# Kernel tuning notes

Measured on AMD Instinct MI355X. Metric: run time of the kernel, lower is better.

The kernel has to match this reference:

```python
import jax, jax.numpy as jnp
from jax import lax
import numpy as np

WINDOW_SIZES = (5, 9, 15)
BASE_LOWER, BASE_UPPER = 0.05, 0.2

def _conv3x3(x, w, b):
    # NCHW / OIHW, stride 1, SAME zero padding (torch Conv2d padding=1)
    y = lax.conv_general_dilated(x, w, (1, 1), 'SAME',
                                 dimension_numbers=('NCHW', 'OIHW', 'NCHW'))
    return y + b.reshape(1, -1, 1, 1)

def _leaky(x):
    return jnp.where(x >= 0, x, 0.2 * x)

def _box_mean(f, win):
    # Depthwise uniform box filter with reflect padding == mean over unfold patches.
    B, C, H, W = f.shape
    pad = win // 2
    fp = jnp.pad(f, ((0, 0), (0, 0), (pad, pad), (pad, pad)), mode='reflect')
    k = jnp.full((C, 1, win, win), 1.0 / (win * win), f.dtype)
    return lax.conv_general_dilated(fp, k, (1, 1), 'VALID',
                                    dimension_numbers=('NCHW', 'OIHW', 'NCHW'),
                                    feature_group_count=C)

def _std_map(features, win):
    m = _box_mean(features, win)                      # E[x]
    m2 = _box_mean(features * features, win)          # E[x^2]
    var = jnp.maximum(m2 - m * m, 0.0)                # == mean((x - mean)^2)
    std = jnp.sqrt(var + 1e-8)                        # [B, C, H, W]
    return jnp.mean(std, axis=1, keepdims=True)       # [B, 1, H, W]

def _forward(x, conv1_w, conv1_b, conv2_w, conv2_b, conv3_w, conv3_b,
             channel_weights, fusion_w, fusion_b):
    # feature extractor: 4 -> 32 -> 16 -> 8
    f = _leaky(_conv3x3(x, conv1_w, conv1_b))
    f = _leaky(_conv3x3(f, conv2_w, conv2_b))
    f = _conv3x3(f, conv3_w, conv3_b)                 # [B, 8, H, W]

    maps = [_std_map(f, w) for w in WINDOW_SIZES]
    multi = jnp.concatenate(maps, axis=1)             # [B, 3, H, W]
    # 1x1 conv fusion (3 -> 1)
    fused = jnp.einsum('bshw,os->bohw', multi, fusion_w[:, :, 0, 0]) \
            + fusion_b.reshape(1, -1, 1, 1)           # [B, 1, H, W]

    # adaptive thresholds (torch.std is unbiased -> ddof=1)
    global_std = jnp.std(x, axis=(2, 3), keepdims=True, ddof=1)   # [B, 4, 1, 1]
    global_factor = jnp.clip(global_std * 5.0, 0.5, 2.0)
    lower = BASE_LOWER * global_factor
    upper = BASE_UPPER * global_factor
    cw = jax.nn.softmax(channel_weights).reshape(1, -1, 1, 1)
    channel_std = jnp.std(x * cw, axis=(2, 3), keepdims=True, ddof=1)
    channel_factor = jnp.clip(channel_std * 2.0, 0.8, 1.2)
    lower = lower * channel_factor                    # [B, 4, 1, 1]
    upper = upper * channel_factor

    ns = jnp.clip((fused - lower) / (upper - lower), 0.0, 1.0)  # broadcasts to [B,4,H,W]
    return jax.nn.sigmoid(6.0 * ns - 3.0)

def setup_inputs() -> dict:
    key = jax.random.key(0)
    ks = jax.random.split(key, 10)
    B, C, H, W = 4, 4, 1024, 1024
    def w_init(k, shape):
        fan_in = shape[1] * shape[2] * shape[3]
        return jax.random.normal(k, shape, jnp.float32) / np.float32(np.sqrt(fan_in))
    return {
        'x': jax.random.uniform(ks[0], (B, C, H, W), jnp.float32),
        'conv1_w': w_init(ks[1], (32, 4, 3, 3)),
        'conv1_b': jax.random.normal(ks[2], (32,), jnp.float32) * 0.01,
        'conv2_w': w_init(ks[3], (16, 32, 3, 3)),
        'conv2_b': jax.random.normal(ks[4], (16,), jnp.float32) * 0.01,
        'conv3_w': w_init(ks[5], (8, 16, 3, 3)),
        'conv3_b': jax.random.normal(ks[6], (8,), jnp.float32) * 0.01,
        'channel_weights': jnp.ones((4,), jnp.float32) / 4.0,
        'fusion_w': w_init(ks[7], (1, 3, 1, 1)),
        'fusion_b': jax.random.normal(ks[8], (1,), jnp.float32) * 0.01,
    }

def reference(x, conv1_w, conv1_b, conv2_w, conv2_b, conv3_w, conv3_b,
              channel_weights, fusion_w, fusion_b):
    return _forward(x, conv1_w, conv1_b, conv2_w, conv2_b, conv3_w, conv3_b,
                    channel_weights, fusion_w, fusion_b)
```

## Files before the change

### kernel.cpp

```cpp
#include <hip/hip_runtime.h>
#include <math.h>

#define H 1024
#define W 1024
#define HW (H * W)

typedef _Float16 half8 __attribute__((ext_vector_type(8)));
typedef _Float16 half4 __attribute__((ext_vector_type(4)));
typedef _Float16 h2 __attribute__((ext_vector_type(2)));
typedef float f32x4 __attribute__((ext_vector_type(4)));
typedef unsigned uint4v __attribute__((ext_vector_type(4)));

__device__ __forceinline__ float fast_sqrtf(float x) { return __builtin_amdgcn_sqrtf(x); }
__device__ __forceinline__ float fast_expf(float x) { return __builtin_amdgcn_exp2f(x * 1.44269504088896340736f); }

__device__ __forceinline__ h2 pkrtz(float a, float b) {
    return __builtin_bit_cast(h2, __builtin_amdgcn_cvt_pkrtz(a, b));
}

__global__ __launch_bounds__(256) void stats_partial(const float* __restrict__ x,
                                                     double* __restrict__ part) {
    int blk = blockIdx.x;
    int bc = blk >> 5;
    int j = blk & 31;
    const float* p = x + (size_t)bc * HW + (size_t)j * (HW / 32);
    int tid = threadIdx.x;
    double s = 0.0, q = 0.0;
    const float4* p4 = (const float4*)p;
    for (int i = tid; i < (HW / 32) / 4; i += 256) {
        float4 v = p4[i];
        s += (double)v.x + (double)v.y + (double)v.z + (double)v.w;
        q += (double)v.x * v.x + (double)v.y * v.y + (double)v.z * v.z + (double)v.w * v.w;
    }
    __shared__ double ls[256], lq[256];
    ls[tid] = s;
    lq[tid] = q;
    __syncthreads();
    for (int ofs = 128; ofs > 0; ofs >>= 1) {
        if (tid < ofs) { ls[tid] += ls[tid + ofs]; lq[tid] += lq[tid + ofs]; }
        __syncthreads();
    }
    if (tid == 0) {
        part[blk * 2] = ls[0];
        part[blk * 2 + 1] = lq[0];
    }
}

__global__ __launch_bounds__(256) void stats_final_prep(const double* __restrict__ part,
                                                        const float* __restrict__ chw,
                                                        const float* __restrict__ w1,
                                                        const float* __restrict__ w2,
                                                        const float* __restrict__ w3,
                                                        float* __restrict__ stats,
                                                        _Float16* __restrict__ w1a,
                                                        _Float16* __restrict__ w3f,
                                                        _Float16* __restrict__ w2bh) {
    int tid = threadIdx.x;
    __shared__ float cw[4];
    if (tid == 0) {
        float m = fmaxf(fmaxf(chw[0], chw[1]), fmaxf(chw[2], chw[3]));
        float e0 = expf(chw[0] - m), e1 = expf(chw[1] - m);
        float e2 = expf(chw[2] - m), e3 = expf(chw[3] - m);
        float s = e0 + e1 + e2 + e3;
        cw[0] = e0 / s; cw[1] = e1 / s; cw[2] = e2 / s; cw[3] = e3 / s;
    }
    __syncthreads();
    if (tid < 16) {
        double s = 0.0, q = 0.0;
        for (int j = 0; j < 32; j++) {
            s += part[(tid * 32 + j) * 2];
            q += part[(tid * 32 + j) * 2 + 1];
        }
        double n = (double)HW;
        double var = (q - s * s / n) / (n - 1.0);
        if (var < 0) var = 0;
        float gs = (float)sqrt(var);
        int c = tid & 3;
        float gf = fminf(fmaxf(gs * 5.0f, 0.5f), 2.0f);
        float cf = fminf(fmaxf(gs * cw[c] * 2.0f, 0.8f), 1.2f);
        stats[tid * 2] = 0.05f * gf * cf;
        stats[tid * 2 + 1] = 0.20f * gf * cf;
    }
    for (int i = tid; i < 256; i += 256) {
        int s = i >> 6, l = i & 63;
        int c = s >> 1, h = s & 1;
        int m = l & 15, cg = l >> 4;
        int co = h * 16 + m;
#pragma unroll
        for (int j = 0; j < 8; j++) {
            int k = c * 32 + cg * 8 + j;
            float v = 0.f;
            if (k < 36) {
                int t = k >> 2, ci = k & 3;
                v = w1[(co * 4 + ci) * 9 + t];
            }
            w1a[i * 8 + j] = (_Float16)v;
        }
    }
    for (int idx = tid; idx < 576; idx += 256) {
        int t = idx >> 6, l = idx & 63;
        int co = l & 15, cg = l >> 4;
#pragma unroll
        for (int j = 0; j < 8; j++) {
            int ci = cg * 8 + j;
            w2bh[idx * 8 + j] = (_Float16)w2[(co * 32 + ci) * 9 + t];
        }
    }
    for (int idx = tid; idx < 384; idx += 256) {
        int t = idx >> 6, l = idx & 63;
        int ky = t / 2, grp = t & 1;
        int co = l & 15, bq = l >> 4;
#pragma unroll
        for (int j = 0; j < 8; j++) {
            int k = bq * 8 + j;
            float v = 0.f;
            if (co < 8) {
                if (grp == 0) {
                    int kxp = k >> 4, ci = k & 15;
                    v = w3[((co * 16 + ci) * 3 + ky) * 3 + kxp];
                } else if (k < 16) {
                    v = w3[((co * 16 + k) * 3 + ky) * 3 + 2];
                }
            }
            w3f[idx * 8 + j] = (_Float16)v;
        }
    }
}

__global__ __launch_bounds__(256, 5) void conv12_mfma(const float* __restrict__ x,
                                                      const _Float16* __restrict__ w1a,
                                                      const float* __restrict__ b1,
                                                      const _Float16* __restrict__ wbh,
                                                      const float* __restrict__ b2,
                                                      _Float16* __restrict__ f2n,
                                                      size_t f2n_bstride, int batch0) {
    __shared__ __align__(16) char smem[30656];
    char* f1t = smem;
    unsigned* xp = (unsigned*)(smem + 27200);
    int tid = threadIdx.x;
    int lane = tid & 63;
    int wid = tid >> 6;
    int bx = blockIdx.x * 32, by = blockIdx.y * 8;
    int n = lane & 15, cg = lane >> 4;
    int m = lane & 15, b = lane >> 4;
    const float* xb = x + (size_t)(batch0 + blockIdx.z) * 4 * HW;
    _Float16* f2nb = f2n + (size_t)blockIdx.z * f2n_bstride;

    {
        int idx = tid;
        int r = tid / 36, c = tid - r * 36, plane = 0;
#pragma unroll
        for (int it = 0; it < 4; ++it) {
            if (idx < 864) {
                int gy = by + r - 2, gx = bx + c - 2;
                float v0 = 0.f, v1 = 0.f;
                if ((unsigned)gy < H && (unsigned)gx < W) {
                    const float* pp = xb + (size_t)(2 * plane) * HW + gy * W + gx;
                    v0 = pp[0];
                    v1 = pp[HW];
                }
                xp[idx] = __builtin_bit_cast(unsigned, pkrtz(v0, v1));
            }
            idx += 256;
            c += 4; if (c >= 36) { c -= 36; r += 1; }
            r += 7; if (r >= 12) { r -= 12; plane += 1; }
        }
    }

    half8 Wf00 = *(const half8*)(w1a + (0 * 64 + lane) * 8);
    half8 Wf01 = *(const half8*)(w1a + (1 * 64 + lane) * 8);
    half8 Wf10 = *(const half8*)(w1a + (2 * 64 + lane) * 8);
    half8 Wf11 = *(const half8*)(w1a + (3 * 64 + lane) * 8);
    float bias1[8];
#pragma unroll
    for (int h = 0; h < 2; h++)
#pragma unroll
        for (int j = 0; j < 4; j++)
            bias1[h * 4 + j] = b1[h * 16 + cg * 4 + j];
    half8 Bh[9];
#pragma unroll
    for (int t = 0; t < 9; t++)
        Bh[t] = *(const half8*)(wbh + (t * 64 + lane) * 8);
    f32x4 binit;
#pragma unroll
    for (int j = 0; j < 4; j++) binit[j] = b2[b * 4 + j];

    int t0 = 2 * cg, t1 = 2 * cg + 1;
    int dy0 = (t0 * 11) >> 5, dx0 = t0 - 3 * dy0;
    int dy1 = (t1 * 11) >> 5, dx1 = t1 - 3 * dy1;
    int off0 = dy0 * 36 + dx0, off1 = dy1 * 36 + dx1;
    __syncthreads();

#pragma unroll 1
    for (int tt = wid; tt < 22; tt += 4) {
        int p = tt * 16 + n;
        bool valid = p < 340;
        int pc = valid ? p : 339;
        int ry = pc / 34, cx = pc - ry * 34;
        int gy = by + ry - 1, gx = bx + cx - 1;
        bool ok = ((unsigned)gy < H) && ((unsigned)gx < W);
        int base = ry * 36 + cx;
        uint4v uv;
        uv.x = xp[base + off0];
        uv.y = xp[432 + base + off0];
        uv.z = xp[base + off1];
        uv.w = xp[432 + base + off1];
        half8 Xh0 = __builtin_bit_cast(half8, uv);
        half8 Xh1 = {0, 0, 0, 0, 0, 0, 0, 0};
        if (cg == 0) {
            uint4v uw = {0, 0, 0, 0};
            uw.x = xp[base + 74];
            uw.y = xp[432 + base + 74];
            Xh1 = __builtin_bit_cast(half8, uw);
        }
        f32x4 d0, d1;
#pragma unroll
        for (int j = 0; j < 4; j++) { d0[j] = bias1[j]; d1[j] = bias1[4 + j]; }
        d0 = __builtin_amdgcn_mfma_f32_16x16x32_f16(Wf00, Xh0, d0, 0, 0, 0);
        d0 = __builtin_amdgcn_mfma_f32_16x16x32_f16(Wf10, Xh1, d0, 0, 0, 0);
        d1 = __builtin_amdgcn_mfma_f32_16x16x32_f16(Wf01, Xh0, d1, 0, 0, 0);
        d1 = __builtin_amdgcn_mfma_f32_16x16x32_f16(Wf11, Xh1, d1, 0, 0, 0);
        if (valid) {
            char* pxb = f1t + ry * 2720 + cx * 80;
#pragma unroll
            for (int h = 0; h < 2; h++) {
                f32x4 d = h ? d1 : d0;
                half4 hq;
#pragma unroll
                for (int j = 0; j < 4; j++) {
                    float v = d[j];
                    v = fmaxf(v, 0.2f * v);
                    v = ok ? v : 0.f;
                    hq[j] = (_Float16)v;
                }
                *(half4*)(pxb + (h * 4 + cg) * 8) = hq;
            }
        }
    }
    __syncthreads();

    int wx = wid & 1, wy = wid >> 1;
    f32x4 acc2[4];
#pragma unroll
    for (int r = 0; r < 4; r++) acc2[r] = binit;
#pragma unroll
    for (int iy = 0; iy < 6; iy++) {
        int f1row = wy * 4 + iy;
        half8 ah[3];
#pragma unroll
        for (int kx = 0; kx < 3; kx++) {
            int pxi = wx * 16 + m + kx;
            ah[kx] = *(const half8*)(f1t + f1row * 2720 + pxi * 80 + b * 16);
        }
#pragma unroll
        for (int kx = 0; kx < 3; kx++) {
#pragma unroll
            for (int ry = 0; ry < 4; ry++) {
                if (ry >= iy - 2 && ry <= iy) {
                    const int t = (iy - ry) * 3 + kx;
                    acc2[ry] = __builtin_amdgcn_mfma_f32_16x16x32_f16(Bh[t], ah[kx], acc2[ry], 0, 0, 0);
                }
            }
        }
    }

    int x0 = bx + wx * 16 + m;
    int y0 = by + wy * 4;
    int co_off = b * 4;
#pragma unroll
    for (int ry = 0; ry < 4; ry++) {
        half4 hq;
#pragma unroll
        for (int j = 0; j < 4; j++) {
            float v = acc2[ry][j];
            v = fmaxf(v, 0.2f * v);
            hq[j] = (_Float16)v;
        }
        *(half4*)(f2nb + ((size_t)(y0 + ry) * W + x0) * 16 + co_off) = hq;
    }
}

__global__ __launch_bounds__(256) void conv3_mfma(const _Float16* __restrict__ f2n,
                                                  size_t f2n_bstride, int batch0,
                                                  const _Float16* __restrict__ w3f,
                                                  const float* __restrict__ bias,
                                                  _Float16* __restrict__ f3all) {
    __shared__ __align__(16) char st[10 * 34 * 40];
    int tid = threadIdx.x;
    int lane = tid & 63;
    int wid = tid >> 6;
    int bx = blockIdx.x * 32, by = blockIdx.y * 8;
    const _Float16* f2nb = f2n + (size_t)blockIdx.z * f2n_bstride;
    _Float16* f3 = f3all + (size_t)(batch0 + blockIdx.z) * 8 * HW;

    for (int idx = tid; idx < 680; idx += 256) {
        int c0 = idx & 1;
        int rp = idx >> 1;
        int r = rp / 34, p = rp - r * 34;
        int gy = by + r - 1, gx = bx + p - 1;
        half8 v = {0, 0, 0, 0, 0, 0, 0, 0};
        if ((unsigned)gy < H && (unsigned)gx < W)
            v = *(const half8*)(f2nb + ((size_t)gy * W + gx) * 16 + c0 * 8);
        *(half8*)(st + r * 1360 + p * 40 + c0 * 16) = v;
    }

    half8 F0[3], F1[3];
#pragma unroll
    for (int ky = 0; ky < 3; ky++) {
        F0[ky] = *(const half8*)(w3f + ((ky * 2 + 0) * 64 + lane) * 8);
        F1[ky] = *(const half8*)(w3f + ((ky * 2 + 1) * 64 + lane) * 8);
    }
    int m = lane & 15, b = lane >> 4;
    int halfco = b & 1, kxp = b >> 1;
    int wx = wid & 1, wy = wid >> 1;
    float bc = (m < 8) ? bias[m] : 0.f;
    f32x4 acc[4];
#pragma unroll
    for (int r = 0; r < 4; r++) acc[r] = (f32x4){bc, bc, bc, bc};
    int pA = wx * 16 + m + kxp;
    int pB = wx * 16 + m + 2;
    __syncthreads();

#pragma unroll
    for (int iy = 0; iy < 6; iy++) {
        const char* rp = st + (wy * 4 + iy) * 1360;
        half8 ka_h = *(const half8*)(rp + pA * 40 + halfco * 16);
        half8 kb_h = *(const half8*)(rp + pB * 40 + halfco * 16);
#pragma unroll
        for (int ry = 0; ry < 4; ry++) {
            if (ry >= iy - 2 && ry <= iy) {
                const int ky = iy - ry;
                acc[ry] = __builtin_amdgcn_mfma_f32_16x16x32_f16(ka_h, F0[ky], acc[ry], 0, 0, 0);
                acc[ry] = __builtin_amdgcn_mfma_f32_16x16x32_f16(kb_h, F1[ky], acc[ry], 0, 0, 0);
            }
        }
    }

    if (m < 8) {
#pragma unroll
        for (int ry = 0; ry < 4; ry++) {
            int y = by + wy * 4 + ry;
            half4 hv = {(_Float16)acc[ry][0], (_Float16)acc[ry][1],
                        (_Float16)acc[ry][2], (_Float16)acc[ry][3]};
            *(half4*)(f3 + (size_t)m * HW + (size_t)y * W + bx + wx * 16 + b * 4) = hv;
        }
    }
}

__global__ __launch_bounds__(256) void stdfuse_fused(const _Float16* __restrict__ f3all,
                                                     const float* __restrict__ fw,
                                                     const float* __restrict__ fb,
                                                     const float* __restrict__ stats,
                                                     float* __restrict__ out) {
    __shared__ __align__(16) _Float16 raw[46 * 50];
    __shared__ __align__(16) _Float16 hsqh[3][46 * 68];
    __shared__ int rowOff[46];
    __shared__ int gxcol[46];
    int tid = threadIdx.x;
    int xq = tid & 15, yp = tid >> 4;
    int bx = blockIdx.x * 32, by = blockIdx.y * 32;
    int batch = blockIdx.z;
    const _Float16* f3 = f3all + (size_t)batch * 8 * HW;

    if (tid < 46) {
        int gy = by + tid - 7;
        gy = gy < 0 ? -gy : (gy > 1023 ? 2046 - gy : gy);
        rowOff[tid] = gy * W;
        int gx = bx + tid - 7;
        gx = gx < 0 ? -gx : (gx > 1023 ? 2046 - gx : gx);
        gxcol[tid] = gx;
    }
    __syncthreads();

    int goffB[9];
    int laddB[9];
    const bool k8 = tid < 68;
#pragma unroll
    for (int k = 0; k < 9; k++) {
        int idx = tid + k * 256;
        int idc = idx < 2116 ? idx : 2115;
        int r = idc / 46, c = idc - r * 46;
        goffB[k] = (rowOff[r] + gxcol[c]) * 2;
        laddB[k] = (r * 50 + c) * 2;
    }

    float wwin[3] = {fw[0] * 0.125f, fw[1] * 0.125f, fw[2] * 0.125f};
    float part[4] = {0.f, 0.f, 0.f, 0.f};

    unsigned short stg[9];
    {
        const char* src = (const char*)f3;
#pragma unroll
        for (int k = 0; k < 8; k++) stg[k] = *(const unsigned short*)(src + goffB[k]);
        stg[8] = k8 ? *(const unsigned short*)(src + goffB[8]) : (unsigned short)0;
    }

    for (int z = 0; z < 8; z++) {
        char* rb = (char*)raw;
#pragma unroll
        for (int k = 0; k < 8; k++) *(unsigned short*)(rb + laddB[k]) = stg[k];
        if (k8) *(unsigned short*)(rb + laddB[8]) = stg[8];

        if (z < 7) {
            const char* nsrc = (const char*)(f3 + (size_t)(z + 1) * HW);
#pragma unroll
            for (int k = 0; k < 8; k++) stg[k] = *(const unsigned short*)(nsrc + goffB[k]);
            if (k8) stg[8] = *(const unsigned short*)(nsrc + goffB[8]);
        }
        __syncthreads();

        for (int idx = tid; idx < 736; idx += 256) {
            int r = idx >> 4, xh = idx & 15;
            const _Float16* rp = raw + r * 50 + 2 * xh;
            float v[16], w[16];
#pragma unroll
            for (int k = 0; k < 8; k++) {
                h2 p = *(const h2*)(rp + 2 * k);
                v[2 * k] = (float)p[0]; v[2 * k + 1] = (float)p[1];
            }
#pragma unroll
            for (int k = 0; k < 16; k++) w[k] = v[k] * v[k];
            float ms = v[6] + v[7] + v[8] + v[9];
            float mq = w[6] + w[7] + w[8] + w[9];
            float sA5 = v[5] + ms, sB5 = ms + v[10];
            float qA5 = w[5] + mq, qB5 = mq + w[10];
            float sA9 = sA5 + v[3] + v[4] + v[10] + v[11];
            float sB9 = sB5 + v[4] + v[5] + v[11] + v[12];
            float qA9 = qA5 + w[3] + w[4] + w[10] + w[11];
            float qB9 = qB5 + w[4] + w[5] + w[11] + w[12];
            float sA15 = sA9 + v[0] + v[1] + v[2] + v[12] + v[13] + v[14];
            float sB15 = sB9 + v[1] + v[2] + v[3] + v[13] + v[14] + v[15];
            float qA15 = qA9 + w[0] + w[1] + w[2] + w[12] + w[13] + w[14];
            float qB15 = qB9 + w[1] + w[2] + w[3] + w[13] + w[14] + w[15];
            int ho = r * 68 + 4 * xh;
            *(half4*)&hsqh[0][ho] = (half4){(_Float16)sA5,  (_Float16)sB5,  (_Float16)qA5,  (_Float16)qB5};
            *(half4*)&hsqh[1][ho] = (half4){(_Float16)sA9,  (_Float16)sB9,  (_Float16)qA9,  (_Float16)qB9};
            *(half4*)&hsqh[2][ho] = (half4){(_Float16)sA15, (_Float16)sB15, (_Float16)qA15, (_Float16)qB15};
        }
        __syncthreads();

#pragma unroll
        for (int wi = 0; wi < 3; wi++) {
            const int wlen = (wi == 0) ? 5 : ((wi == 1) ? 9 : 15);
            const int r0 = 2 * yp + 7 - (wlen >> 1);
            const float inv = 1.0f / (float)(wlen * wlen);
            const float ww = wwin[wi];
            const _Float16* basep = &hsqh[wi][4 * xq];
            half4 first = *(const half4*)(basep + r0 * 68);
            half4 e = first;
            half4 o = *(const half4*)(basep + (r0 + 1) * 68);
#pragma unroll
            for (int k = 2; k + 1 < wlen; k += 2) {
                e += *(const half4*)(basep + (r0 + k) * 68);
                o += *(const half4*)(basep + (r0 + k + 1) * 68);
            }
            e += *(const half4*)(basep + (r0 + wlen - 1) * 68);
            half4 tot = e + o;
            half4 last = *(const half4*)(basep + (r0 + wlen) * 68);
            half4 sh = tot - first + last;
            float sA0 = (float)tot[0], sB0 = (float)tot[1];
            float qA0 = (float)tot[2], qB0 = (float)tot[3];
            float sA1 = (float)sh[0],  sB1 = (float)sh[1];
            float qA1 = (float)sh[2],  qB1 = (float)sh[3];
            float mA0 = sA0 * inv, m2A0 = qA0 * inv;
            part[0] += ww * fast_sqrtf(fmaxf(m2A0 - mA0 * mA0, 0.f) + 1e-8f);
            float mB0 = sB0 * inv, m2B0 = qB0 * inv;
            part[1] += ww * fast_sqrtf(fmaxf(m2B0 - mB0 * mB0, 0.f) + 1e-8f);
            float mA1 = sA1 * inv, m2A1 = qA1 * inv;
            part[2] += ww * fast_sqrtf(fmaxf(m2A1 - mA1 * mA1, 0.f) + 1e-8f);
            float mB1 = sB1 * inv, m2B1 = qB1 * inv;
            part[3] += ww * fast_sqrtf(fmaxf(m2B1 - mB1 * mB1, 0.f) + 1e-8f);
        }
    }

    float fb0 = fb[0];
    int gy = by + 2 * yp, gx = bx + 2 * xq;
#pragma unroll
    for (int c = 0; c < 4; c++) {
        float lo = stats[(batch * 4 + c) * 2];
        float up = stats[(batch * 4 + c) * 2 + 1];
        float inv = 1.f / (up - lo);
        float v[4];
#pragma unroll
        for (int p = 0; p < 4; p++) {
            float ns = (part[p] + fb0 - lo) * inv;
            ns = fminf(fmaxf(ns, 0.f), 1.f);
            v[p] = 1.f / (1.f + fast_expf(3.f - 6.f * ns));
        }
        float* plane = out + ((size_t)(batch * 4 + c)) * HW;
        *(float2*)(plane + (size_t)gy * W + gx) = make_float2(v[0], v[1]);
        *(float2*)(plane + (size_t)(gy + 1) * W + gx) = make_float2(v[2], v[3]);
    }
}

extern "C" void kernel_launch(void* const* d_in, const int* in_sizes, int n_in,
                              void* d_out, int out_size, void* d_ws, size_t ws_size,
                              hipStream_t stream) {
    (void)in_sizes; (void)n_in; (void)out_size;
    const float* x = (const float*)d_in[0];
    const float* w1 = (const float*)d_in[1];
    const float* b1 = (const float*)d_in[2];
    const float* w2 = (const float*)d_in[3];
    const float* b2 = (const float*)d_in[4];
    const float* w3 = (const float*)d_in[5];
    const float* b3 = (const float*)d_in[6];
    const float* chw = (const float*)d_in[7];
    const float* fw = (const float*)d_in[8];
    const float* fb = (const float*)d_in[9];
    float* out = (float*)d_out;

    char* ws = (char*)d_ws;
    float* stats = (float*)ws;
    double* part = (double*)(ws + 256);
    _Float16* w1a = (_Float16*)(ws + 8448);
    _Float16* w3f = (_Float16*)(ws + 24832);
    _Float16* w2bh = (_Float16*)(ws + 37120);
    _Float16* f3all = (_Float16*)(ws + 65536);
    _Float16* f2n = (_Float16*)(ws + 67174400);

    const size_t PLANE = (size_t)16 * HW;
    const size_t WIDE_WS = 67174400ULL + 4ULL * PLANE * sizeof(_Float16);
    bool wide = ws_size >= WIDE_WS;

    stats_partial<<<512, 256, 0, stream>>>(x, part);
    stats_final_prep<<<1, 256, 0, stream>>>(part, chw, w1, w2, w3, stats, w1a, w3f, w2bh);

    if (wide) {
        conv12_mfma<<<dim3(32, 128, 4), 256, 0, stream>>>(x, w1a, b1, w2bh, b2, f2n, PLANE, 0);
        conv3_mfma<<<dim3(32, 128, 4), 256, 0, stream>>>(f2n, PLANE, 0, w3f, b3, f3all);
    } else {
        for (int b = 0; b < 4; b++) {
            conv12_mfma<<<dim3(32, 128, 1), 256, 0, stream>>>(x, w1a, b1, w2bh, b2, f2n, 0, b);
            conv3_mfma<<<dim3(32, 128, 1), 256, 0, stream>>>(f2n, 0, b, w3f, b3, f3all);
        }
    }
    stdfuse_fused<<<dim3(32, 32, 4), 256, 0, stream>>>(f3all, fw, fb, stats, out);
}
```

Measured before the change: 326.6 us.

## Process two feature channels per pass with packed half2 box sums

The std-fusion kernel now interleaves two feature channels into one half2 LDS element. It runs four passes over channel pairs instead of eight single-channel passes, computing horizontal window sums with packed fp16 math instead of fp32 conversions. The intent is to halve the syncthreads barriers and LDS passes and use packed ALU throughput. The trade-off is that horizontal sums are now accumulated in fp16, which loses precision, and the LDS footprint roughly doubles for the sum buffer, which can lower occupancy.

```diff
diff --git a/kernel.cpp b/kernel.cpp
--- a/kernel.cpp
+++ b/kernel.cpp
@@ -352,8 +352,8 @@
                                                      const float* __restrict__ fb,
                                                      const float* __restrict__ stats,
                                                      float* __restrict__ out) {
-    __shared__ __align__(16) _Float16 raw[46 * 50];
-    __shared__ __align__(16) _Float16 hsqh[3][46 * 68];
+    __shared__ __align__(16) h2 raw2[46 * 50];
+    __shared__ __align__(16) _Float16 hsqh[3][46 * 132];
     __shared__ int rowOff[46];
     __shared__ int gxcol[46];
     int tid = threadIdx.x;
@@ -373,7 +373,7 @@
     __syncthreads();
 
     int goffB[9];
-    int laddB[9];
+    int laddW[9];
     const bool k8 = tid < 68;
 #pragma unroll
     for (int k = 0; k < 9; k++) {
@@ -381,61 +381,83 @@
         int idc = idx < 2116 ? idx : 2115;
         int r = idc / 46, c = idc - r * 46;
         goffB[k] = (rowOff[r] + gxcol[c]) * 2;
-        laddB[k] = (r * 50 + c) * 2;
+        laddW[k] = r * 50 + c;
     }
 
     float wwin[3] = {fw[0] * 0.125f, fw[1] * 0.125f, fw[2] * 0.125f};
     float part[4] = {0.f, 0.f, 0.f, 0.f};
 
-    unsigned short stg[9];
+    unsigned sa[9], sb[9];
     {
-        const char* src = (const char*)f3;
-#pragma unroll
-        for (int k = 0; k < 8; k++) stg[k] = *(const unsigned short*)(src + goffB[k]);
-        stg[8] = k8 ? *(const unsigned short*)(src + goffB[8]) : (unsigned short)0;
-    }
-
-    for (int z = 0; z < 8; z++) {
-        char* rb = (char*)raw;
-#pragma unroll
-        for (int k = 0; k < 8; k++) *(unsigned short*)(rb + laddB[k]) = stg[k];
-        if (k8) *(unsigned short*)(rb + laddB[8]) = stg[8];
-
-        if (z < 7) {
-            const char* nsrc = (const char*)(f3 + (size_t)(z + 1) * HW);
-#pragma unroll
-            for (int k = 0; k < 8; k++) stg[k] = *(const unsigned short*)(nsrc + goffB[k]);
-            if (k8) stg[8] = *(const unsigned short*)(nsrc + goffB[8]);
+        const char* pa = (const char*)f3;
+        const char* pb = (const char*)(f3 + HW);
+#pragma unroll
+        for (int k = 0; k < 8; k++) {
+            sa[k] = *(const unsigned short*)(pa + goffB[k]);
+            sb[k] = *(const unsigned short*)(pb + goffB[k]);
+        }
+        sa[8] = k8 ? *(const unsigned short*)(pa + goffB[8]) : 0u;
+        sb[8] = k8 ? *(const unsigned short*)(pb + goffB[8]) : 0u;
+    }
+
+    for (int zp = 0; zp < 4; zp++) {
+        unsigned* rb = (unsigned*)raw2;
+#pragma unroll
+        for (int k = 0; k < 8; k++) rb[laddW[k]] = sa[k] | (sb[k] << 16);
+        if (k8) rb[laddW[8]] = sa[8] | (sb[8] << 16);
+
+        if (zp < 3) {
+            const char* na = (const char*)(f3 + (size_t)(2 * zp + 2) * HW);
+            const char* nb = (const char*)(f3 + (size_t)(2 * zp + 3) * HW);
+#pragma unroll
+            for (int k = 0; k < 8; k++) {
+                sa[k] = *(const unsigned short*)(na + goffB[k]);
+                sb[k] = *(const unsigned short*)(nb + goffB[k]);
+            }
+            if (k8) {
+                sa[8] = *(const unsigned short*)(na + goffB[8]);
+                sb[8] = *(const unsigned short*)(nb + goffB[8]);
+            }
         }
         __syncthreads();
 
         for (int idx = tid; idx < 736; idx += 256) {
             int r = idx >> 4, xh = idx & 15;
-            const _Float16* rp = raw + r * 50 + 2 * xh;
-            float v[16], w[16];
-#pragma unroll
-            for (int k = 0; k < 8; k++) {
-                h2 p = *(const h2*)(rp + 2 * k);
-                v[2 * k] = (float)p[0]; v[2 * k + 1] = (float)p[1];
-            }
+            const h2* rp = raw2 + r * 50 + 2 * xh;
+            h2 v[16], w[16];
+#pragma unroll
+            for (int k = 0; k < 16; k++) v[k] = rp[k];
 #pragma unroll
             for (int k = 0; k < 16; k++) w[k] = v[k] * v[k];
-            float ms = v[6] + v[7] + v[8] + v[9];
-            float mq = w[6] + w[7] + w[8] + w[9];
-            float sA5 = v[5] + ms, sB5 = ms + v[10];
-            float qA5 = w[5] + mq, qB5 = mq + w[10];
-            float sA9 = sA5 + v[3] + v[4] + v[10] + v[11];
-            float sB9 = sB5 + v[4] + v[5] + v[11] + v[12];
-            float qA9 = qA5 + w[3] + w[4] + w[10] + w[11];
-            float qB9 = qB5 + w[4] + w[5] + w[11] + w[12];
-            float sA15 = sA9 + v[0] + v[1] + v[2] + v[12] + v[13] + v[14];
-            float sB15 = sB9 + v[1] + v[2] + v[3] + v[13] + v[14] + v[15];
-            float qA15 = qA9 + w[0] + w[1] + w[2] + w[12] + w[13] + w[14];
-            float qB15 = qB9 + w[1] + w[2] + w[3] + w[13] + w[14] + w[15];
-            int ho = r * 68 + 4 * xh;
-            *(half4*)&hsqh[0][ho] = (half4){(_Float16)sA5,  (_Float16)sB5,  (_Float16)qA5,  (_Float16)qB5};
-            *(half4*)&hsqh[1][ho] = (half4){(_Float16)sA9,  (_Float16)sB9,  (_Float16)qA9,  (_Float16)qB9};
-            *(half4*)&hsqh[2][ho] = (half4){(_Float16)sA15, (_Float16)sB15, (_Float16)qA15, (_Float16)qB15};
+            h2 ms = v[6] + v[7] + v[8] + v[9];
+            h2 mq = w[6] + w[7] + w[8] + w[9];
+            h2 sA5 = v[5] + ms, sB5 = ms + v[10];
+            h2 qA5 = w[5] + mq, qB5 = mq + w[10];
+            h2 sA9 = sA5 + v[3] + v[4] + v[10] + v[11];
+            h2 sB9 = sB5 + v[4] + v[5] + v[11] + v[12];
+            h2 qA9 = qA5 + w[3] + w[4] + w[10] + w[11];
+            h2 qB9 = qB5 + w[4] + w[5] + w[11] + w[12];
+            h2 sA15 = sA9 + v[0] + v[1] + v[2] + v[12] + v[13] + v[14];
+            h2 sB15 = sB9 + v[1] + v[2] + v[3] + v[13] + v[14] + v[15];
+            h2 qA15 = qA9 + w[0] + w[1] + w[2] + w[12] + w[13] + w[14];
+            h2 qB15 = qB9 + w[1] + w[2] + w[3] + w[13] + w[14] + w[15];
+            int ho = r * 132 + 8 * xh;
+            uint4v u0, u1, u2;
+            u0.x = __builtin_bit_cast(unsigned, sA5);
+            u0.y = __builtin_bit_cast(unsigned, sB5);
+            u0.z = __builtin_bit_cast(unsigned, qA5);
+            u0.w = __builtin_bit_cast(unsigned, qB5);
+            u1.x = __builtin_bit_cast(unsigned, sA9);
+            u1.y = __builtin_bit_cast(unsigned, sB9);
+            u1.z = __builtin_bit_cast(unsigned, qA9);
+            u1.w = __builtin_bit_cast(unsigned, qB9);
+            u2.x = __builtin_bit_cast(unsigned, sA15);
+            u2.y = __builtin_bit_cast(unsigned, sB15);
+            u2.z = __builtin_bit_cast(unsigned, qA15);
+            u2.w = __builtin_bit_cast(unsigned, qB15);
+            *(uint4v*)&hsqh[0][ho] = u0;
+            *(uint4v*)&hsqh[1][ho] = u1;
+            *(uint4v*)&hsqh[2][ho] = u2;
         }
         __syncthreads();
 
@@ -445,31 +467,30 @@
             const int r0 = 2 * yp + 7 - (wlen >> 1);
             const float inv = 1.0f / (float)(wlen * wlen);
             const float ww = wwin[wi];
-            const _Float16* basep = &hsqh[wi][4 * xq];
-            half4 first = *(const half4*)(basep + r0 * 68);
-            half4 e = first;
-            half4 o = *(const half4*)(basep + (r0 + 1) * 68);
+            const _Float16* basep = &hsqh[wi][8 * xq];
+            half8 first = *(const half8*)(basep + r0 * 132);
+            half8 e = first;
+            half8 o = *(const half8*)(basep + (r0 + 1) * 132);
 #pragma unroll
             for (int k = 2; k + 1 < wlen; k += 2) {
-                e += *(const half4*)(basep + (r0 + k) * 68);
-                o += *(const half4*)(basep + (r0 + k + 1) * 68);
-            }
-            e += *(const half4*)(basep + (r0 + wlen - 1) * 68);
-            half4 tot = e + o;
-            half4 last = *(const half4*)(basep + (r0 + wlen) * 68);
-            half4 sh = tot - first + last;
-            float sA0 = (float)tot[0], sB0 = (float)tot[1];
-            float qA0 = (float)tot[2], qB0 = (float)tot[3];
-            float sA1 = (float)sh[0],  sB1 = (float)sh[1];
-            float qA1 = (float)sh[2],  qB1 = (float)sh[3];
-            float mA0 = sA0 * inv, m2A0 = qA0 * inv;
-            part[0] += ww * fast_sqrtf(fmaxf(m2A0 - mA0 * mA0, 0.f) + 1e-8f);
-            float mB0 = sB0 * inv, m2B0 = qB0 * inv;
-            part[1] += ww * fast_sqrtf(fmaxf(m2B0 - mB0 * mB0, 0.f) + 1e-8f);
-            float mA1 = sA1 * inv, m2A1 = qA1 * inv;
-            part[2] += ww * fast_sqrtf(fmaxf(m2A1 - mA1 * mA1, 0.f) + 1e-8f);
-            float mB1 = sB1 * inv, m2B1 = qB1 * inv;
-            part[3] += ww * fast_sqrtf(fmaxf(m2B1 - mB1 * mB1, 0.f) + 1e-8f);
+                e += *(const half8*)(basep + (r0 + k) * 132);
+                o += *(const half8*)(basep + (r0 + k + 1) * 132);
+            }
+            e += *(const half8*)(basep + (r0 + wlen - 1) * 132);
+            half8 tot = e + o;
+            half8 last = *(const half8*)(basep + (r0 + wlen) * 132);
+            half8 sh = tot - first + last;
+#pragma unroll
+            for (int ch = 0; ch < 2; ch++) {
+                float mA0 = (float)tot[0 + ch] * inv, m2A0 = (float)tot[4 + ch] * inv;
+                part[0] += ww * fast_sqrtf(fmaxf(m2A0 - mA0 * mA0, 0.f) + 1e-8f);
+                float mB0 = (float)tot[2 + ch] * inv, m2B0 = (float)tot[6 + ch] * inv;
+                part[1] += ww * fast_sqrtf(fmaxf(m2B0 - mB0 * mB0, 0.f) + 1e-8f);
+                float mA1 = (float)sh[0 + ch] * inv, m2A1 = (float)sh[4 + ch] * inv;
+                part[2] += ww * fast_sqrtf(fmaxf(m2A1 - mA1 * mA1, 0.f) + 1e-8f);
+                float mB1 = (float)sh[2 + ch] * inv, m2B1 = (float)sh[6 + ch] * inv;
+                part[3] += ww * fast_sqrtf(fmaxf(m2B1 - mB1 * mB1, 0.f) + 1e-8f);
+            }
         }
     }
 
```

After: 392.1 us. 1.2x slower.
